# Optimization experiments

Measured on AMD Instinct MI355X. Metric: run time of the kernel, lower is better.

Reference implementation:

```python
import jax, jax.numpy as jnp
import numpy as np


def setup_inputs() -> dict:
    key = jax.random.key(0)
    k1, k2, k3 = jax.random.split(key, 3)
    N, C, H, W, O = 4, 256, 64, 64, 256
    x = jax.random.normal(k1, (N, C, H, W), jnp.float32)
    # offset per forward signature: [N, H*W, 2*3*3]
    offset = jax.random.normal(k2, (N, H * W, 18), jnp.float32)
    # DeformConv weight [O, C, 3, 3], normal_init std=0.01, bias=False
    weight = jax.random.normal(k3, (O, C, 3, 3), jnp.float32) * 0.01
    return {"x": x, "offset": offset, "weight": weight}


def _deform_conv3x3(x, offset, weight):
    """Deformable conv v1: 3x3, stride 1, padding 1, dilation 1, no bias.
    x: [N,C,H,W]; offset: [N,HW,18] (permuted to [N,18,H,W] as in the module);
    weight: [O,C,3,3].
    """
    N, C, H, W = x.shape
    O = weight.shape[0]
    # module does offset.permute(0,2,1).reshape(N,-1,H,W) -> [N,18,H,W]
    off = offset.transpose(0, 2, 1).reshape(N, 9, 2, H, W)  # (dy,dx) per kernel pos
    dy, dx = off[:, :, 0], off[:, :, 1]                      # [N,9,H,W]

    # base 3x3 kernel offsets (padding=1 keeps the grid centered)
    ky = jnp.array([-1, -1, -1, 0, 0, 0, 1, 1, 1], x.dtype)
    kx = jnp.array([-1, 0, 1, -1, 0, 1, -1, 0, 1], x.dtype)
    hg = jnp.arange(H, dtype=x.dtype)[:, None]  # [H,1]
    wg = jnp.arange(W, dtype=x.dtype)[None, :]  # [1,W]
    py = hg[None, None] + ky[None, :, None, None] + dy  # [N,9,H,W] sample rows
    px = wg[None, None] + kx[None, :, None, None] + dx  # [N,9,H,W] sample cols

    y0 = jnp.floor(py)
    x0 = jnp.floor(px)
    wy = (py - y0)[:, None]  # [N,1,9,H,W]
    wx = (px - x0)[:, None]

    def gather(iy, ix):
        # zero-padded gather: out[n,c,k,h,w] = x[n,c,iy,ix] (0 if out of bounds)
        valid = (iy >= 0) & (iy < H) & (ix >= 0) & (ix < W)
        iyc = jnp.clip(iy, 0, H - 1).astype(jnp.int32)
        ixc = jnp.clip(ix, 0, W - 1).astype(jnp.int32)
        g = jax.vmap(lambda xn, yn, wn: xn[:, yn, wn])(x, iyc, ixc)  # [N,C,9,H,W]
        return g * valid[:, None].astype(x.dtype)

    v00 = gather(y0, x0)
    v01 = gather(y0, x0 + 1)
    v10 = gather(y0 + 1, x0)
    v11 = gather(y0 + 1, x0 + 1)
    # bilinear blend -> sampled columns [N,C,9,H,W]
    val = (v00 * (1 - wy) * (1 - wx) + v01 * (1 - wy) * wx
           + v10 * wy * (1 - wx) + v11 * wy * wx)
    # conv accumulate over channels and kernel positions
    return jnp.einsum('nckhw,ock->nohw', val, weight.reshape(O, C, 9))


def reference(x, offset, weight):
    return _deform_conv3x3(x, offset, weight)
```

## Files before the change

### kernel.cpp

```cpp
#include <hip/hip_runtime.h>
#include <hip/hip_fp16.h>

#define CC 256
#define OO 256
#define HH 64
#define WW 64
#define HWN 4096
#define MPB 32
#define VST 264

typedef _Float16 half8 __attribute__((ext_vector_type(8)));
typedef _Float16 half2v __attribute__((ext_vector_type(2)));
typedef float f32x4 __attribute__((ext_vector_type(4)));

__device__ __forceinline__ half2v u2h(unsigned u) {
  half2v h; __builtin_memcpy(&h, &u, 4); return h;
}
__device__ __forceinline__ unsigned h2u(half2v h) {
  unsigned u; __builtin_memcpy(&u, &h, 4); return u;
}
__device__ __forceinline__ unsigned short f2h(float f) {
  _Float16 h = (_Float16)f;
  unsigned short us; __builtin_memcpy(&us, &h, 2);
  return us;
}
__device__ __forceinline__ unsigned dupu(unsigned short us) {
  return ((unsigned)us << 16) | us;
}
__device__ __forceinline__ unsigned pk2(float a, float b) {
  half2v h = {(_Float16)a, (_Float16)b};
  return h2u(h);
}

__device__ __forceinline__ void vsync() {
  __builtin_amdgcn_sched_barrier(0);
  asm volatile("s_waitcnt lgkmcnt(0)" ::: "memory");
  __builtin_amdgcn_s_barrier();
  __builtin_amdgcn_sched_barrier(0);
}

__global__ __launch_bounds__(256) void prep_kernel(
    const float* __restrict__ x, const float* __restrict__ w,
    _Float16* __restrict__ xt, _Float16* __restrict__ wt) {
  const int bid = blockIdx.x;
  const int tid = threadIdx.x;
  if (bid < 1024) {
    __shared__ float tile[64][65];
    const int n  = bid >> 8;
    const int c0 = ((bid >> 6) & 3) * 64;
    const int s0 = (bid & 63) * 64;
    {
      int r  = tid >> 2;
      int sc = (tid & 3) * 16;
      const float* xp = x + ((size_t)(n * CC + c0 + r)) * HWN + s0 + sc;
      float4 va = *(const float4*)(xp);
      float4 vb = *(const float4*)(xp + 4);
      float4 vc = *(const float4*)(xp + 8);
      float4 vd = *(const float4*)(xp + 12);
      tile[sc + 0][r]  = va.x;  tile[sc + 1][r]  = va.y;
      tile[sc + 2][r]  = va.z;  tile[sc + 3][r]  = va.w;
      tile[sc + 4][r]  = vb.x;  tile[sc + 5][r]  = vb.y;
      tile[sc + 6][r]  = vb.z;  tile[sc + 7][r]  = vb.w;
      tile[sc + 8][r]  = vc.x;  tile[sc + 9][r]  = vc.y;
      tile[sc + 10][r] = vc.z;  tile[sc + 11][r] = vc.w;
      tile[sc + 12][r] = vd.x;  tile[sc + 13][r] = vd.y;
      tile[sc + 14][r] = vd.z;  tile[sc + 15][r] = vd.w;
    }
    __syncthreads();
    {
      int s  = tid >> 2;
      int cg = (tid & 3) * 16;
      uint4 u0, u1;
      u0.x = pk2(tile[s][cg + 0],  tile[s][cg + 1]);
      u0.y = pk2(tile[s][cg + 2],  tile[s][cg + 3]);
      u0.z = pk2(tile[s][cg + 4],  tile[s][cg + 5]);
      u0.w = pk2(tile[s][cg + 6],  tile[s][cg + 7]);
      u1.x = pk2(tile[s][cg + 8],  tile[s][cg + 9]);
      u1.y = pk2(tile[s][cg + 10], tile[s][cg + 11]);
      u1.z = pk2(tile[s][cg + 12], tile[s][cg + 13]);
      u1.w = pk2(tile[s][cg + 14], tile[s][cg + 15]);
      _Float16* op = xt + ((size_t)(n * HWN + s0 + s)) * CC + c0 + cg;
      *(uint4*)(op)     = u0;
      *(uint4*)(op + 8) = u1;
    }
  } else {
    __shared__ _Float16 wrow[9][264];
    const int o = bid - 1024;
    const float* wp = w + (size_t)o * (CC * 9);
    float v[9];
#pragma unroll
    for (int k = 0; k < 9; ++k) v[k] = wp[tid * 9 + k];
#pragma unroll
    for (int k = 0; k < 9; ++k) wrow[k][tid] = (_Float16)v[k];
    __syncthreads();
    for (int r = tid; r < 9 * 64; r += 256) {
      int k  = r >> 6;
      int c4 = (r & 63) * 4;
      *(uint2*)(wt + (size_t)k * (OO * CC) + (size_t)o * CC + c4) =
          *(const uint2*)(&wrow[k][c4]);
    }
  }
}

__global__ __launch_bounds__(512, 4) void deform_mfma_kernel(
    const _Float16* __restrict__ xt,
    const _Float16* __restrict__ wt,
    const float* __restrict__ off,
    float* __restrict__ out) {
  __shared__ __align__(16) _Float16 val_lds[MPB * VST];
  __shared__ ushort4 s_po[MPB * 9];
  __shared__ ushort4 s_pw[MPB * 9];

  const int tid  = threadIdx.x;
  const int lane = tid & 63;
  const int wv   = tid >> 6;
  const int n15  = lane & 15;
  const int quad = lane >> 4;

  const int bx  = blockIdx.x;
  const int xcd = bx & 7;
  const int nb  = xcd >> 1;
  const int hw0 = (((xcd & 1) << 6) | (bx >> 3)) * MPB;

  const int o0 = wv * 32;

  if (tid < MPB * 9) {
    int e = tid;
    int p = e / 9;
    int k = e - p * 9;
    int hw = hw0 + p;
    int h = hw >> 6, w = hw & 63;
    size_t ob = ((size_t)(nb * HWN + hw)) * 18 + 2 * k;
    float2 d = *(const float2*)(off + ob);
    float py = (float)(h + k / 3 - 1) + d.x;
    float px = (float)(w + k % 3 - 1) + d.y;
    float fy = floorf(py), fx = floorf(px);
    int iy = (int)fy, ix = (int)fx;
    float wy = py - fy, wx = px - fx;
    float my0 = ((unsigned)iy       < (unsigned)HH) ? 1.f : 0.f;
    float my1 = ((unsigned)(iy + 1) < (unsigned)HH) ? 1.f : 0.f;
    float mx0 = ((unsigned)ix       < (unsigned)WW) ? 1.f : 0.f;
    float mx1 = ((unsigned)(ix + 1) < (unsigned)WW) ? 1.f : 0.f;
    int iy0 = min(max(iy, 0), HH - 1), iy1 = min(max(iy + 1, 0), HH - 1);
    int ix0 = min(max(ix, 0), WW - 1), ix1 = min(max(ix + 1, 0), WW - 1);
    s_po[e] = make_ushort4((unsigned short)(iy0 * WW + ix0),
                           (unsigned short)(iy0 * WW + ix1),
                           (unsigned short)(iy1 * WW + ix0),
                           (unsigned short)(iy1 * WW + ix1));
    s_pw[e] = make_ushort4(f2h((1.f - wy) * (1.f - wx) * my0 * mx0),
                           f2h((1.f - wy) * wx         * my0 * mx1),
                           f2h(wy         * (1.f - wx) * my1 * mx0),
                           f2h(wy         * wx         * my1 * mx1));
  }

  f32x4 acc[2][2];
#pragma unroll
  for (int a = 0; a < 2; ++a)
#pragma unroll
    for (int b = 0; b < 2; ++b) acc[a][b] = (f32x4){0.f, 0.f, 0.f, 0.f};

  const _Float16* xb = xt + (size_t)nb * HWN * CC;
  const int j    = tid & 31;
  const int slot = tid >> 5;

  auto sample_tap = [&](int kk) {
#pragma unroll
    for (int i = 0; i < 2; ++i) {
      int p = i * 16 + slot;
      int idx = p * 9 + kk;
      ushort4 o4 = s_po[idx];
      ushort4 hw4 = s_pw[idx];
      half2v w00 = u2h(dupu(hw4.x)), w01 = u2h(dupu(hw4.y));
      half2v w10 = u2h(dupu(hw4.z)), w11 = u2h(dupu(hw4.w));
      const _Float16* cb = xb + (size_t)j * 8;
      uint4 v00 = *(const uint4*)(cb + (size_t)o4.x * CC);
      uint4 v01 = *(const uint4*)(cb + (size_t)o4.y * CC);
      uint4 v10 = *(const uint4*)(cb + (size_t)o4.z * CC);
      uint4 v11 = *(const uint4*)(cb + (size_t)o4.w * CC);
      uint4 r;
      r.x = h2u(u2h(v00.x) * w00 + u2h(v01.x) * w01 + u2h(v10.x) * w10 + u2h(v11.x) * w11);
      r.y = h2u(u2h(v00.y) * w00 + u2h(v01.y) * w01 + u2h(v10.y) * w10 + u2h(v11.y) * w11);
      r.z = h2u(u2h(v00.z) * w00 + u2h(v01.z) * w01 + u2h(v10.z) * w10 + u2h(v11.z) * w11);
      r.w = h2u(u2h(v00.w) * w00 + u2h(v01.w) * w01 + u2h(v10.w) * w10 + u2h(v11.w) * w11);
      *(uint4*)(val_lds + p * VST + j * 8) = r;
    }
  };

  __syncthreads();
  sample_tap(0);
  vsync();

  for (int k = 0; k < 9; ++k) {
    const _Float16* wb = wt + ((size_t)(k * OO + o0)) * CC;
    half8 bfr[2][8];
#pragma unroll
    for (int nt = 0; nt < 2; ++nt)
#pragma unroll
      for (int ksg = 0; ksg < 8; ++ksg)
        bfr[nt][ksg] = *(const half8*)(wb + (size_t)(nt * 16 + n15) * CC + ksg * 32 + quad * 8);
    __builtin_amdgcn_sched_barrier(0);

#pragma unroll
    for (int ksg = 0; ksg < 8; ++ksg) {
      half8 afr[2];
#pragma unroll
      for (int mt = 0; mt < 2; ++mt)
        afr[mt] = *(const half8*)(val_lds + (mt * 16 + n15) * VST + ksg * 32 + quad * 8);
#pragma unroll
      for (int mt = 0; mt < 2; ++mt)
#pragma unroll
        for (int nt = 0; nt < 2; ++nt)
          acc[mt][nt] = __builtin_amdgcn_mfma_f32_16x16x32_f16(
              afr[mt], bfr[nt][ksg], acc[mt][nt], 0, 0, 0);
    }

    vsync();
    if (k < 8) sample_tap(k + 1);
    vsync();
  }

#pragma unroll
  for (int mt = 0; mt < 2; ++mt)
#pragma unroll
    for (int nt = 0; nt < 2; ++nt) {
      int o  = o0 + nt * 16 + n15;
      int px = hw0 + mt * 16 + quad * 4;
      *(f32x4*)(out + ((size_t)nb * OO + o) * HWN + px) = acc[mt][nt];
    }
}

extern "C" void kernel_launch(void* const* d_in, const int* in_sizes, int n_in,
                              void* d_out, int out_size, void* d_ws, size_t ws_size,
                              hipStream_t stream) {
  const float* x   = (const float*)d_in[0];
  const float* off = (const float*)d_in[1];
  const float* w   = (const float*)d_in[2];
  float* out = (float*)d_out;

  _Float16* wt = (_Float16*)d_ws;
  _Float16* xt = wt + 589824;

  prep_kernel<<<1024 + 256, 256, 0, stream>>>(x, w, xt, wt);
  deform_mfma_kernel<<<512, 512, 0, stream>>>(xt, wt, off, out);
}
```

Baseline: 152.6 us.

## Double-buffer sampled LDS tile to overlap next-tap gather with MFMA

Doubles the LDS buffer that holds the sampled bilinear values, so the gather for tap k+1 writes into the other buffer while MFMAs consume the current one. This removes one of the two barriers per tap. Weight fragments are issued before the barrier, and empty asm barriers split their consumption into two halves to influence scheduling. In exchange it doubles LDS use for that buffer, which could lower occupancy, and the scheduler may still serialize the gather and the MFMAs.

```diff
diff --git a/kernel.cpp b/kernel.cpp
--- a/kernel.cpp
+++ b/kernel.cpp
@@ -8,6 +8,7 @@
 #define HWN 4096
 #define MPB 32
 #define VST 264
+#define VOFF (MPB * VST)
 
 typedef _Float16 half8 __attribute__((ext_vector_type(8)));
 typedef _Float16 half2v __attribute__((ext_vector_type(2)));
@@ -107,7 +108,7 @@
     const _Float16* __restrict__ wt,
     const float* __restrict__ off,
     float* __restrict__ out) {
-  __shared__ __align__(16) _Float16 val_lds[MPB * VST];
+  __shared__ __align__(16) _Float16 val_lds[2 * VOFF];
   __shared__ ushort4 s_po[MPB * 9];
   __shared__ ushort4 s_pw[MPB * 9];
 
@@ -163,7 +164,7 @@
   const int j    = tid & 31;
   const int slot = tid >> 5;
 
-  auto sample_tap = [&](int kk) {
+  auto sample_tap = [&](int kk, int bb) {
 #pragma unroll
     for (int i = 0; i < 2; ++i) {
       int p = i * 16 + slot;
@@ -182,41 +183,58 @@
       r.y = h2u(u2h(v00.y) * w00 + u2h(v01.y) * w01 + u2h(v10.y) * w10 + u2h(v11.y) * w11);
       r.z = h2u(u2h(v00.z) * w00 + u2h(v01.z) * w01 + u2h(v10.z) * w10 + u2h(v11.z) * w11);
       r.w = h2u(u2h(v00.w) * w00 + u2h(v01.w) * w01 + u2h(v10.w) * w10 + u2h(v11.w) * w11);
-      *(uint4*)(val_lds + p * VST + j * 8) = r;
+      *(uint4*)(val_lds + bb * VOFF + p * VST + j * 8) = r;
     }
   };
 
   __syncthreads();
-  sample_tap(0);
-  vsync();
-
+  sample_tap(0, 0);
+
+  int cur = 0;
   for (int k = 0; k < 9; ++k) {
+    const int nxt = cur ^ 1;
+
     const _Float16* wb = wt + ((size_t)(k * OO + o0)) * CC;
-    half8 bfr[2][8];
-#pragma unroll
-    for (int nt = 0; nt < 2; ++nt)
-#pragma unroll
-      for (int ksg = 0; ksg < 8; ++ksg)
-        bfr[nt][ksg] = *(const half8*)(wb + (size_t)(nt * 16 + n15) * CC + ksg * 32 + quad * 8);
-    __builtin_amdgcn_sched_barrier(0);
-
+    half8 b0[8], b1[8];
 #pragma unroll
     for (int ksg = 0; ksg < 8; ++ksg) {
+      b0[ksg] = *(const half8*)(wb + (size_t)(n15)      * CC + ksg * 32 + quad * 8);
+      b1[ksg] = *(const half8*)(wb + (size_t)(16 + n15) * CC + ksg * 32 + quad * 8);
+    }
+
+    vsync();
+
+    if (k < 8) sample_tap(k + 1, nxt);
+
+    asm volatile("" : "+v"(b0[0]), "+v"(b0[1]), "+v"(b0[2]), "+v"(b0[3]),
+                      "+v"(b1[0]), "+v"(b1[1]), "+v"(b1[2]), "+v"(b1[3]));
+#pragma unroll
+    for (int ksg = 0; ksg < 4; ++ksg) {
       half8 afr[2];
 #pragma unroll
       for (int mt = 0; mt < 2; ++mt)
-        afr[mt] = *(const half8*)(val_lds + (mt * 16 + n15) * VST + ksg * 32 + quad * 8);
+        afr[mt] = *(const half8*)(val_lds + cur * VOFF + (mt * 16 + n15) * VST + ksg * 32 + quad * 8);
+      acc[0][0] = __builtin_amdgcn_mfma_f32_16x16x32_f16(afr[0], b0[ksg], acc[0][0], 0, 0, 0);
+      acc[0][1] = __builtin_amdgcn_mfma_f32_16x16x32_f16(afr[0], b1[ksg], acc[0][1], 0, 0, 0);
+      acc[1][0] = __builtin_amdgcn_mfma_f32_16x16x32_f16(afr[1], b0[ksg], acc[1][0], 0, 0, 0);
+      acc[1][1] = __builtin_amdgcn_mfma_f32_16x16x32_f16(afr[1], b1[ksg], acc[1][1], 0, 0, 0);
+    }
+
+    asm volatile("" : "+v"(b0[4]), "+v"(b0[5]), "+v"(b0[6]), "+v"(b0[7]),
+                      "+v"(b1[4]), "+v"(b1[5]), "+v"(b1[6]), "+v"(b1[7]));
+#pragma unroll
+    for (int ksg = 4; ksg < 8; ++ksg) {
+      half8 afr[2];
 #pragma unroll
       for (int mt = 0; mt < 2; ++mt)
-#pragma unroll
-        for (int nt = 0; nt < 2; ++nt)
-          acc[mt][nt] = __builtin_amdgcn_mfma_f32_16x16x32_f16(
-              afr[mt], bfr[nt][ksg], acc[mt][nt], 0, 0, 0);
-    }
-
-    vsync();
-    if (k < 8) sample_tap(k + 1);
-    vsync();
+        afr[mt] = *(const half8*)(val_lds + cur * VOFF + (mt * 16 + n15) * VST + ksg * 32 + quad * 8);
+      acc[0][0] = __builtin_amdgcn_mfma_f32_16x16x32_f16(afr[0], b0[ksg], acc[0][0], 0, 0, 0);
+      acc[0][1] = __builtin_amdgcn_mfma_f32_16x16x32_f16(afr[0], b1[ksg], acc[0][1], 0, 0, 0);
+      acc[1][0] = __builtin_amdgcn_mfma_f32_16x16x32_f16(afr[1], b0[ksg], acc[1][0], 0, 0, 0);
+      acc[1][1] = __builtin_amdgcn_mfma_f32_16x16x32_f16(afr[1], b1[ksg], acc[1][1], 0, 0, 0);
+    }
+
+    cur = nxt;
   }
 
 #pragma unroll
```

Measured after the change: 157.9 us. +3.5%, slower.
